# Kernel optimization log

Hardware: AMD Instinct MI355X
Metric: run time of the kernel (lower is better)

## Reference

```python
import jax, jax.numpy as jnp
import numpy as np

# TripletSTDP hyperparameters (match torch defaults / init_kwargs)
TAU_PLUS = 20.0
TAU_MINUS = 20.0
TAU_X = 101.0
TAU_Y = 114.0
A_PLUS = 0.005
A_MINUS = 0.00525
A_TRIP_PLUS = 0.0001
A_TRIP_MINUS = 0.0001
DT = 1.0

B, T, N_PRE, N_POST = 32, 512, 1024, 1024


def setup_inputs() -> dict:
    key = jax.random.key(0)
    k1, k2, k3 = jax.random.split(key, 3)
    pre_spikes = jax.random.uniform(k1, (B, T, N_PRE), dtype=jnp.float32)
    post_spikes = jax.random.uniform(k2, (B, T, N_POST), dtype=jnp.float32)
    weights = jax.random.uniform(k3, (N_PRE, N_POST), dtype=jnp.float32)
    return {"pre_spikes": pre_spikes, "post_spikes": post_spikes, "weights": weights}


def reference(pre_spikes, post_spikes, weights):
    batch, time_steps, n_pre = pre_spikes.shape
    n_post = post_spikes.shape[-1]
    d_plus = jnp.exp(jnp.asarray(-DT / TAU_PLUS, dtype=pre_spikes.dtype))
    d_x = jnp.exp(jnp.asarray(-DT / TAU_X, dtype=pre_spikes.dtype))
    d_minus = jnp.exp(jnp.asarray(-DT / TAU_MINUS, dtype=pre_spikes.dtype))
    d_y = jnp.exp(jnp.asarray(-DT / TAU_Y, dtype=pre_spikes.dtype))
    inv_b = 1.0 / batch

    def step(carry, xs):
        r1, r2, o1, o2, wu = carry
        pre_t, post_t = xs  # [B, n_pre], [B, n_post]
        r1 = r1 * d_plus
        r2 = r2 * d_x
        o1 = o1 * d_minus
        o2 = o2 * d_y
        # LTP: (a_plus*r1 + a_tp*r1*r2) outer post_t, mean over batch
        wu = wu + jnp.einsum('bp,bq->pq', A_PLUS * r1 + A_TRIP_PLUS * (r1 * r2), post_t) * inv_b
        # LTD: pre_t outer (a_minus*o1 + a_tm*o1*o2), mean over batch, negated
        wu = wu - jnp.einsum('bp,bq->pq', pre_t, A_MINUS * o1 + A_TRIP_MINUS * (o1 * o2)) * inv_b
        return (r1 + pre_t, r2 + pre_t, o1 + post_t, o2 + post_t, wu), None

    init = (
        jnp.zeros((batch, n_pre), dtype=pre_spikes.dtype),
        jnp.zeros((batch, n_pre), dtype=pre_spikes.dtype),
        jnp.zeros((batch, n_post), dtype=post_spikes.dtype),
        jnp.zeros((batch, n_post), dtype=post_spikes.dtype),
        jnp.zeros_like(weights),
    )
    xs = (jnp.swapaxes(pre_spikes, 0, 1), jnp.swapaxes(post_spikes, 0, 1))  # [T,B,*]
    (r1, r2, o1, o2, wu), _ = jax.lax.scan(step, init, xs)
    return wu / time_steps
```

## Files before the change

### kernel.cpp

```cpp
#include <hip/hip_runtime.h>
#include <cstdint>
#include <cmath>

#define BDIM 256

constexpr int Bsz = 32;
constexpr int Tt  = 512;
constexpr int Nn  = 1024;
constexpr int SEG = 8;
constexpr int SLEN = 64;
constexpr int SPLITS = 8;
constexpr int NKT = (2 * Bsz * Tt / 32) / SPLITS;
constexpr float A_PLUS  = 0.005f;
constexpr float A_MINUS = 0.00525f;
constexpr float A_TP    = 0.0001f;
constexpr float A_TM    = 0.0001f;

typedef __attribute__((ext_vector_type(8))) short short8;
typedef __attribute__((ext_vector_type(4))) float float4v;

__device__ __forceinline__ unsigned short f2bf(float f) {
  unsigned u = __float_as_uint(f);
  u += 0x7fffu + ((u >> 16) & 1u);
  return (unsigned short)(u >> 16);
}

__global__ __launch_bounds__(BDIM, 4) void trace_kernel(
    const float* __restrict__ pre, const float* __restrict__ post,
    unsigned short* __restrict__ Abuf, unsigned short* __restrict__ Bbuf,
    float d_plus, float d_x, float d_minus, float d_y)
{
  int nb   = blockIdx.x & 31;
  int b    = (blockIdx.x >> 5) & 31;
  int side = blockIdx.x >> 10;
  int tid  = threadIdx.x;
  int seg  = tid >> 5;
  int nl   = tid & 31;
  int n    = nb * 32 + nl;

  const float* sp = (side ? post : pre) + (size_t)b * Tt * Nn + n;
  float da = side ? d_minus : d_plus;
  float db = side ? d_y     : d_x;
  float c1 = side ? -A_MINUS : A_PLUS;
  float c2 = side ? -A_TM    : A_TP;
  unsigned short* dbuf = side ? Bbuf : Abuf;
  int sw = (nl >> 1) & 3;
  int t0 = seg * SLEN;

  __shared__ __align__(16) unsigned short op[SEG][2][32][32];
  float* lds1 = (float*)&op[0][0][0][0];
  float* lds2 = lds1 + SEG * 32;

  float s[SLEN];
#pragma unroll
  for (int j = 0; j < SLEN; ++j) s[j] = sp[(size_t)(t0 + j) * Nn];
#pragma unroll
  for (int j = 0; j < SLEN; ++j) asm volatile("" : "+v"(s[j]));

  float l1 = 0.f, l2 = 0.f;
#pragma unroll
  for (int j = 0; j < SLEN; ++j) {
    l1 = l1 * da + s[j];
    l2 = l2 * db + s[j];
  }

  float dL1 = da, dL2 = db;
#pragma unroll
  for (int q = 0; q < 6; ++q) { dL1 *= dL1; dL2 *= dL2; }

  lds1[seg * 32 + nl] = l1; lds2[seg * 32 + nl] = l2;
  __syncthreads();
  float tr1 = 0.f, tr2 = 0.f;
#pragma unroll
  for (int m = 0; m < SEG - 1; ++m) {
    if (m < seg) {
      tr1 = tr1 * dL1 + lds1[m * 32 + nl];
      tr2 = tr2 * dL2 + lds2[m * 32 + nl];
    }
  }
  __syncthreads();

  int wid = tid >> 6, lane = tid & 63;

#pragma unroll
  for (int r = 0; r < 2; ++r) {
#pragma unroll
    for (int g2 = 0; g2 < 2; ++g2) {
      short8 w0[2], w1[2];
#pragma unroll
      for (int j = 0; j < 16; ++j) {
        float sv = s[r * 32 + g2 * 16 + j];
        tr1 *= da; tr2 *= db;
        float tv = c1 * tr1 + c2 * (tr1 * tr2);
        unsigned short bs = f2bf(sv);
        unsigned short bt = f2bf(tv);
        unsigned short h0 = side ? bs : bt;
        unsigned short h1 = side ? bt : bs;
        w0[j >> 3][j & 7] = (short)h0;
        w1[j >> 3][j & 7] = (short)h1;
        tr1 += sv; tr2 += sv;
      }
#pragma unroll
      for (int i = 0; i < 2; ++i) {
        int slot = g2 * 2 + i;
        *(short8*)&op[seg][0][nl][(slot ^ sw) * 8] = w0[i];
        *(short8*)&op[seg][1][nl][(slot ^ sw) * 8] = w1[i];
      }
    }
    __syncthreads();

    const unsigned short* opb = &op[0][0][0][0];
#pragma unroll
    for (int i = 0; i < 4; ++i) {
      int rid = wid * 4 + i;
      int sg  = rid >> 1;
      int dX  = rid & 1;
      size_t kt = (size_t)(dX * 512 + b * 16 + sg * 2 + r);
      size_t ge = (kt * 8 + (size_t)(nb >> 2)) * 4096 + (size_t)(nb & 3) * 1024;
#pragma unroll
      for (int h = 0; h < 2; ++h) {
        *(short8*)(dbuf + ge + h * 512 + lane * 8) =
            *(const short8*)(opb + (size_t)rid * 1024 + h * 512 + lane * 8);
      }
    }
    if (r == 0) __syncthreads();
  }
}

#define GLL(gp, lp)                                                         \
  __builtin_amdgcn_global_load_lds(                                         \
      (const __attribute__((address_space(1))) unsigned int*)(gp),          \
      (__attribute__((address_space(3))) unsigned int*)(lp), 16, 0, 0)

#define WAITCNT_VM8 0xF78
#define WAITCNT_VM4 0xF74
#define WAITCNT_VM0 0xF70

__global__ __launch_bounds__(BDIM) void gemm_kernel(
    const unsigned short* __restrict__ Abuf, const unsigned short* __restrict__ Bbuf,
    float* __restrict__ partials)
{
  __shared__ unsigned short smem[3 * 8192];
  int tid  = threadIdx.x;
  int s    = blockIdx.x & 7;
  int tile = blockIdx.x >> 3;
  int pt   = tile & 7;
  int qt   = tile >> 3;

  float4v acc[4][4];
#pragma unroll
  for (int i = 0; i < 4; ++i)
#pragma unroll
    for (int j = 0; j < 4; ++j) acc[i][j] = (float4v){0.f, 0.f, 0.f, 0.f};

  int wid = tid >> 6, lane = tid & 63;
  int wr = wid >> 1, wc = wid & 1;
  int rA = wr * 64 + (lane & 15);
  int rB = wc * 64 + (lane & 15);
  int kg = (((lane >> 4) ^ ((lane >> 1) & 3)) * 8);

  const unsigned short* ga = Abuf + ((size_t)(s * NKT) * 8 + pt) * 4096 + tid * 8;
  const unsigned short* gb = Bbuf + ((size_t)(s * NKT) * 8 + qt) * 4096 + tid * 8;

#define ISSUE(kt_) do {                                                     \
    unsigned short* sb_ = smem + ((kt_) % 3) * 8192;                        \
    const unsigned short* a_ = ga + (size_t)(kt_) * 8 * 4096;               \
    const unsigned short* b_ = gb + (size_t)(kt_) * 8 * 4096;               \
    GLL(a_,        sb_ + tid * 8);                                          \
    GLL(a_ + 2048, sb_ + 2048 + tid * 8);                                   \
    GLL(b_,        sb_ + 4096 + tid * 8);                                   \
    GLL(b_ + 2048, sb_ + 6144 + tid * 8);                                   \
  } while (0)

  ISSUE(0);
  ISSUE(1);

  for (int kt = 0; kt < NKT; ++kt) {
    if (kt + 2 < NKT) {
      ISSUE(kt + 2);
      __builtin_amdgcn_s_waitcnt(WAITCNT_VM8);
    } else if (kt + 2 == NKT) {
      __builtin_amdgcn_s_waitcnt(WAITCNT_VM4);
    } else {
      __builtin_amdgcn_s_waitcnt(WAITCNT_VM0);
    }
    __builtin_amdgcn_s_barrier();

    const unsigned short* sb = smem + (kt % 3) * 8192;
    short8 af[4], bfv[4];
#pragma unroll
    for (int mi = 0; mi < 4; ++mi)
      af[mi] = *(const short8*)(sb + (rA + mi * 16) * 32 + kg);
#pragma unroll
    for (int ni = 0; ni < 4; ++ni)
      bfv[ni] = *(const short8*)(sb + 4096 + (rB + ni * 16) * 32 + kg);
#pragma unroll
    for (int mi = 0; mi < 4; ++mi)
#pragma unroll
      for (int ni = 0; ni < 4; ++ni)
        acc[mi][ni] = __builtin_amdgcn_mfma_f32_16x16x32_bf16(af[mi], bfv[ni], acc[mi][ni], 0, 0, 0);
  }

  float* po = partials + (size_t)s * Nn * Nn;
#pragma unroll
  for (int mi = 0; mi < 4; ++mi)
#pragma unroll
    for (int r = 0; r < 4; ++r) {
      int row = pt * 128 + wr * 64 + mi * 16 + (lane >> 4) * 4 + r;
#pragma unroll
      for (int ni = 0; ni < 4; ++ni) {
        int col = qt * 128 + wc * 64 + ni * 16 + (lane & 15);
        po[(size_t)row * Nn + col] = acc[mi][ni][r];
      }
    }
#undef ISSUE
}

__global__ __launch_bounds__(BDIM) void reduce_kernel(
    const float4v* __restrict__ partials, float4v* __restrict__ out, int S, float scale)
{
  size_t i = (size_t)blockIdx.x * BDIM + threadIdx.x;
  float4v v = (float4v){0.f, 0.f, 0.f, 0.f};
  for (int s = 0; s < S; ++s) v += partials[(size_t)s * (Nn * Nn / 4) + i];
  out[i] = v * scale;
}

extern "C" void kernel_launch(void* const* d_in, const int* in_sizes, int n_in,
                              void* d_out, int out_size, void* d_ws, size_t ws_size,
                              hipStream_t stream)
{
  const float* pre  = (const float*)d_in[0];
  const float* post = (const float*)d_in[1];
  float4v* out = (float4v*)d_out;
  char* ws = (char*)d_ws;

  size_t sizeAB = (size_t)2 * Bsz * Tt * Nn * 2;

  float* partials = (float*)ws;
  unsigned short* Abuf = (unsigned short*)(ws + (size_t)SPLITS * Nn * Nn * 4);
  unsigned short* Bbuf = (unsigned short*)(ws + (size_t)SPLITS * Nn * Nn * 4 + sizeAB);

  float d_plus  = expf(-1.0f / 20.0f);
  float d_x     = expf(-1.0f / 101.0f);
  float d_minus = expf(-1.0f / 20.0f);
  float d_y     = expf(-1.0f / 114.0f);

  trace_kernel<<<2 * Bsz * Nn / 32, BDIM, 0, stream>>>(
      pre, post, Abuf, Bbuf, d_plus, d_x, d_minus, d_y);
  gemm_kernel<<<64 * SPLITS, BDIM, 0, stream>>>(Abuf, Bbuf, partials);
  reduce_kernel<<<(Nn * Nn / 4) / BDIM, BDIM, 0, stream>>>(
      (const float4v*)partials, out, SPLITS, 1.0f / (float)(Bsz * Tt));
}
```

Before: 244.0 us.

## Enlarge GEMM tile to 256x128 with 512 threads, double-buffered two-k-step stages

The GEMM now uses 512-thread blocks, each covering a 256x128 output tile, so each B tile loaded into LDS is shared by twice as many rows. Each pipeline stage loads two k-steps into one of two LDS buffers, giving fewer barriers per unit of work. MFMA sections are wrapped in s_setprio to favour math issue. The cost is fewer blocks (256 total) with more LDS each, and a shallower pipeline, which may reduce latency hiding and occupancy.

After: 251.9 us. +3.2%, slower.

```diff
diff --git a/kernel.cpp b/kernel.cpp
--- a/kernel.cpp
+++ b/kernel.cpp
@@ -11,6 +11,7 @@
 constexpr int SLEN = 64;
 constexpr int SPLITS = 8;
 constexpr int NKT = (2 * Bsz * Tt / 32) / SPLITS;
+constexpr int NT  = NKT / 2;
 constexpr float A_PLUS  = 0.005f;
 constexpr float A_MINUS = 0.00525f;
 constexpr float A_TP    = 0.0001f;
@@ -132,20 +133,19 @@
       (const __attribute__((address_space(1))) unsigned int*)(gp),          \
       (__attribute__((address_space(3))) unsigned int*)(lp), 16, 0, 0)
 
-#define WAITCNT_VM8 0xF78
-#define WAITCNT_VM4 0xF74
+#define WAITCNT_VM6 0xF76
 #define WAITCNT_VM0 0xF70
 
-__global__ __launch_bounds__(BDIM) void gemm_kernel(
+__global__ __launch_bounds__(512) void gemm_kernel(
     const unsigned short* __restrict__ Abuf, const unsigned short* __restrict__ Bbuf,
     float* __restrict__ partials)
 {
-  __shared__ unsigned short smem[3 * 8192];
+  __shared__ unsigned short smem[2 * 24576];
   int tid  = threadIdx.x;
   int s    = blockIdx.x & 7;
   int tile = blockIdx.x >> 3;
-  int pt   = tile & 7;
-  int qt   = tile >> 3;
+  int pt   = tile & 3;
+  int qt   = tile >> 2;
 
   float4v acc[4][4];
 #pragma unroll
@@ -159,46 +159,53 @@
   int rB = wc * 64 + (lane & 15);
   int kg = (((lane >> 4) ^ ((lane >> 1) & 3)) * 8);
 
-  const unsigned short* ga = Abuf + ((size_t)(s * NKT) * 8 + pt) * 4096 + tid * 8;
-  const unsigned short* gb = Bbuf + ((size_t)(s * NKT) * 8 + qt) * 4096 + tid * 8;
-
-#define ISSUE(kt_) do {                                                     \
-    unsigned short* sb_ = smem + ((kt_) % 3) * 8192;                        \
-    const unsigned short* a_ = ga + (size_t)(kt_) * 8 * 4096;               \
-    const unsigned short* b_ = gb + (size_t)(kt_) * 8 * 4096;               \
-    GLL(a_,        sb_ + tid * 8);                                          \
-    GLL(a_ + 2048, sb_ + 2048 + tid * 8);                                   \
-    GLL(b_,        sb_ + 4096 + tid * 8);                                   \
-    GLL(b_ + 2048, sb_ + 6144 + tid * 8);                                   \
+  const unsigned short* gaBase = Abuf + ((size_t)(s * NKT) * 8 + pt * 2) * 4096 + tid * 8;
+  const unsigned short* gbBase = Bbuf + ((size_t)(s * NKT) * 8 + qt) * 4096 + tid * 8;
+
+#define ISSUE(t_) do {                                                          \
+    unsigned short* sb_ = smem + ((t_) & 1) * 24576;                            \
+    GLL(gaBase + ((size_t)(2*(t_)    ) * 8 + 0) * 4096, sb_ +         tid * 8); \
+    GLL(gaBase + ((size_t)(2*(t_)    ) * 8 + 1) * 4096, sb_ +  4096 + tid * 8); \
+    GLL(gaBase + ((size_t)(2*(t_) + 1) * 8 + 0) * 4096, sb_ +  8192 + tid * 8); \
+    GLL(gaBase + ((size_t)(2*(t_) + 1) * 8 + 1) * 4096, sb_ + 12288 + tid * 8); \
+    GLL(gbBase + ((size_t)(2*(t_)    ) * 8    ) * 4096, sb_ + 16384 + tid * 8); \
+    GLL(gbBase + ((size_t)(2*(t_) + 1) * 8    ) * 4096, sb_ + 20480 + tid * 8); \
   } while (0)
 
   ISSUE(0);
-  ISSUE(1);
-
-  for (int kt = 0; kt < NKT; ++kt) {
-    if (kt + 2 < NKT) {
-      ISSUE(kt + 2);
-      __builtin_amdgcn_s_waitcnt(WAITCNT_VM8);
-    } else if (kt + 2 == NKT) {
-      __builtin_amdgcn_s_waitcnt(WAITCNT_VM4);
+
+  for (int t = 0; t < NT; ++t) {
+    __builtin_amdgcn_s_barrier();
+    if (t + 1 < NT) {
+      ISSUE(t + 1);
+      __builtin_amdgcn_s_waitcnt(WAITCNT_VM6);
     } else {
       __builtin_amdgcn_s_waitcnt(WAITCNT_VM0);
     }
     __builtin_amdgcn_s_barrier();
 
-    const unsigned short* sb = smem + (kt % 3) * 8192;
-    short8 af[4], bfv[4];
-#pragma unroll
-    for (int mi = 0; mi < 4; ++mi)
-      af[mi] = *(const short8*)(sb + (rA + mi * 16) * 32 + kg);
-#pragma unroll
-    for (int ni = 0; ni < 4; ++ni)
-      bfv[ni] = *(const short8*)(sb + 4096 + (rB + ni * 16) * 32 + kg);
-#pragma unroll
-    for (int mi = 0; mi < 4; ++mi)
+    const unsigned short* sb = smem + (t & 1) * 24576;
+#pragma unroll
+    for (int ktl = 0; ktl < 2; ++ktl) {
+      const unsigned short* sa  = sb + ktl * 8192;
+      const unsigned short* sbB = sb + 16384 + ktl * 4096;
+      short8 af[4], bfv[4];
+#pragma unroll
+      for (int mi = 0; mi < 4; ++mi) {
+        int r = rA + mi * 16;
+        af[mi] = *(const short8*)(sa + (r >> 7) * 4096 + (r & 127) * 32 + kg);
+      }
 #pragma unroll
       for (int ni = 0; ni < 4; ++ni)
-        acc[mi][ni] = __builtin_amdgcn_mfma_f32_16x16x32_bf16(af[mi], bfv[ni], acc[mi][ni], 0, 0, 0);
+        bfv[ni] = *(const short8*)(sbB + (rB + ni * 16) * 32 + kg);
+      __builtin_amdgcn_s_setprio(1);
+#pragma unroll
+      for (int mi = 0; mi < 4; ++mi)
+#pragma unroll
+        for (int ni = 0; ni < 4; ++ni)
+          acc[mi][ni] = __builtin_amdgcn_mfma_f32_16x16x32_bf16(af[mi], bfv[ni], acc[mi][ni], 0, 0, 0);
+      __builtin_amdgcn_s_setprio(0);
+    }
   }
 
   float* po = partials + (size_t)s * Nn * Nn;
@@ -206,7 +213,7 @@
   for (int mi = 0; mi < 4; ++mi)
 #pragma unroll
     for (int r = 0; r < 4; ++r) {
-      int row = pt * 128 + wr * 64 + mi * 16 + (lane >> 4) * 4 + r;
+      int row = pt * 256 + wr * 64 + mi * 16 + (lane >> 4) * 4 + r;
 #pragma unroll
       for (int ni = 0; ni < 4; ++ni) {
         int col = qt * 128 + wc * 64 + ni * 16 + (lane & 15);
@@ -247,7 +254,7 @@
 
   trace_kernel<<<2 * Bsz * Nn / 32, BDIM, 0, stream>>>(
       pre, post, Abuf, Bbuf, d_plus, d_x, d_minus, d_y);
-  gemm_kernel<<<64 * SPLITS, BDIM, 0, stream>>>(Abuf, Bbuf, partials);
+  gemm_kernel<<<32 * SPLITS, 512, 0, stream>>>(Abuf, Bbuf, partials);
   reduce_kernel<<<(Nn * Nn / 4) / BDIM, BDIM, 0, stream>>>(
       (const float4v*)partials, out, SPLITS, 1.0f / (float)(Bsz * Tt));
 }
```
